# Kernel tuning notes

Measured on AMD Instinct MI355X. Metric: run time of the kernel, lower is better.

## Reference

```python
import jax, jax.numpy as jnp
import numpy as np
from jax import lax

B, L, H, E, V = 16, 128, 1024, 512, 32000
MAX_LENGTH = 128
SOS_INDEX = 1
NUM_LAYERS = 2


def setup_inputs() -> dict:
    key = jax.random.key(0)
    ks = jax.random.split(key, 16)
    inp = {}
    inp['input_tensor'] = jax.random.randint(ks[0], (B, L), 0, V)
    inp['target_tensor'] = jax.random.randint(ks[1], (B, L), 0, V)
    inp['true_sample'] = 1
    s = lambda k, shape, fan: jax.random.normal(k, shape, jnp.float32) / np.float32(np.sqrt(fan))
    inp['embedding'] = jax.random.normal(ks[2], (V, E), jnp.float32) * 0.02
    inp['enc_W'] = s(ks[3], (E, H), E)
    inp['enc_b'] = jnp.zeros((H,), jnp.float32)
    inp['Wih0'] = s(ks[4], (E, 3 * H), E)
    inp['Whh0'] = s(ks[5], (H, 3 * H), H)
    inp['bih0'] = jnp.zeros((3 * H,), jnp.float32)
    inp['bhh0'] = jnp.zeros((3 * H,), jnp.float32)
    inp['Wih1'] = s(ks[6], (H, 3 * H), H)
    inp['Whh1'] = s(ks[7], (H, 3 * H), H)
    inp['bih1'] = jnp.zeros((3 * H,), jnp.float32)
    inp['bhh1'] = jnp.zeros((3 * H,), jnp.float32)
    inp['W_out'] = s(ks[8], (2 * H, V), 2 * H)
    inp['b_out'] = jnp.zeros((V,), jnp.float32)
    return inp


def _gru_cell(x, h, Wih, Whh, bih, bhh):
    gx = x @ Wih + bih
    gh = h @ Whh + bhh
    xr, xz, xn = jnp.split(gx, 3, axis=-1)
    hr, hz, hn = jnp.split(gh, 3, axis=-1)
    r = jax.nn.sigmoid(xr + hr)
    z = jax.nn.sigmoid(xz + hz)
    n = jnp.tanh(xn + r * hn)
    return (1.0 - z) * n + z * h


def _forward(input_tensor, true_sample, embedding, enc_W, enc_b,
             Wih0, Whh0, bih0, bhh0, Wih1, Whh1, bih1, bhh1, W_out, b_out):
    batch_size, input_length = input_tensor.shape
    target_length = input_length
    # Encoder: embed + per-timestep projection -> [B, L, H]
    enc_emb = embedding[input_tensor]
    enc_hidden = jnp.tanh(enc_emb @ enc_W + enc_b)
    enc_hidden_t = jnp.transpose(enc_hidden, (1, 0, 2))  # [L, B, H]
    # Pad at the front to max_length (mirrors the copy loop)
    encoder_outputs = jnp.zeros((MAX_LENGTH, batch_size, H), enc_hidden.dtype)
    encoder_outputs = encoder_outputs.at[MAX_LENGTH - input_length:].set(enc_hidden_t)
    # Decoder initial hidden: last encoder state stacked over layers
    h_init = enc_hidden_t[-1]  # [B, H]
    # NOTE: original never updates decoder_input inside the loop -> constant SOS
    x0 = jnp.broadcast_to(embedding[SOS_INDEX], (batch_size, E))
    inv_sqrt_h = np.float32(1.0 / np.sqrt(H))

    def step(carry, _):
        h0, h1 = carry
        h0 = _gru_cell(x0, h0, Wih0, Whh0, bih0, bhh0)
        h1 = _gru_cell(h0, h1, Wih1, Whh1, bih1, bhh1)
        scores = jnp.einsum('bh,lbh->bl', h1, encoder_outputs) * inv_sqrt_h
        attn = jax.nn.softmax(scores, axis=-1)
        ctx = jnp.einsum('bl,lbh->bh', attn, encoder_outputs)
        logits = jnp.concatenate([h1, ctx], axis=-1) @ W_out + b_out
        return (h0, h1), jax.nn.sigmoid(logits)

    _, probs = lax.scan(step, (h_init, h_init), None, length=target_length)
    decoder_outputs = jnp.transpose(probs, (1, 0, 2))  # [B, T, V]
    # Scalar gather: p[b,w] = decoder_outputs[b, w, input_tensor[b, w]]
    out_probabilities = jnp.take_along_axis(decoder_outputs, input_tensor[..., None], axis=2)[..., 0]
    target = jnp.full(input_tensor.shape, np.float32(int(true_sample)), jnp.float32)
    p = jnp.clip(out_probabilities, 1e-12, 1.0 - 1e-7)
    bce = -(target * jnp.log(p) + (1.0 - target) * jnp.log1p(-p))
    loss = jnp.mean(bce) / np.float32(batch_size)
    return loss, out_probabilities


def reference(input_tensor, target_tensor, true_sample, embedding, enc_W, enc_b,
              Wih0, Whh0, bih0, bhh0, Wih1, Whh1, bih1, bhh1, W_out, b_out):
    return _forward(input_tensor, true_sample, embedding, enc_W, enc_b,
                    Wih0, Whh0, bih0, bhh0, Wih1, Whh1, bih1, bhh1, W_out, b_out)
```

## Files before the change

### kernel.cpp

```cpp
#include <hip/hip_runtime.h>
#include <math.h>

#define BB 16
#define LL 128
#define HH 1024
#define EE 512
#define VV 32000
#define G3 3072
#define NBLK 256

__device__ __forceinline__ float sigmoidf_(float x){ return 1.0f/(1.0f+expf(-x)); }

__global__ void k_rowidx(const int* __restrict__ inp, int* __restrict__ idx){
  int r = blockIdx.x*256 + threadIdx.x;
  if (r < 2048){ int l = r >> 4, b = r & 15; idx[r] = inp[b*LL + l]; }
}

template<int ACT, int KK>
__global__ __launch_bounds__(256) void k_gemm(const float* __restrict__ A, const int* __restrict__ rowidx,
                       const float* __restrict__ Bm, const float* __restrict__ bias,
                       float* __restrict__ C, int N){
  constexpr int KS = (KK==512)?9:10;
  __shared__ float As[32*KK];
  const int tid = threadIdx.x;
  const int r0 = blockIdx.x*32;
  const int c  = blockIdx.y*512 + (tid<<1);
  for (int i = tid; i < 32*KK; i += 256){
    int rr = i >> KS;
    int row = r0 + rr;
    int arow = rowidx ? rowidx[row] : row;
    int kk = i - (rr<<KS);
    As[i] = A[(size_t)arow*KK + kk];
  }
  __syncthreads();
  float2 acc[32];
  #pragma unroll
  for (int r=0;r<32;r++){ acc[r].x=0.f; acc[r].y=0.f; }
  for (int k=0;k<KK;k++){
    const float2 w = *(const float2*)(Bm + (size_t)k*N + c);
    #pragma unroll
    for (int r=0;r<32;r++){
      float a = As[(r<<KS)+k];
      acc[r].x = fmaf(a,w.x,acc[r].x);
      acc[r].y = fmaf(a,w.y,acc[r].y);
    }
  }
  const float2 bv = *(const float2*)(bias + c);
  #pragma unroll
  for (int r=0;r<32;r++){
    float x = acc[r].x + bv.x, y = acc[r].y + bv.y;
    if (ACT==1){ x = tanhf(x); y = tanhf(y); }
    *(float2*)(C + (size_t)(r0+r)*N + c) = make_float2(x,y);
  }
}

__global__ __launch_bounds__(256,1) void k_chains(
    const float* enclast, float* H0all, float* H1all,
    const float* __restrict__ Whh0, const float* __restrict__ Whh1,
    const float* __restrict__ Wih0, const float* __restrict__ Wih1,
    const float* __restrict__ emb,
    const float* __restrict__ bih0, const float* __restrict__ bhh0,
    const float* __restrict__ bhh1, const float* __restrict__ bih1,
    int* flags, int* go)
{
  __shared__ float w0l[12][1024];
  __shared__ float w1l[12][1024];
  __shared__ float wil[12][1024];
  const int tid  = threadIdx.x;
  const int lane = tid & 63;
  const int bc   = tid >> 6;
  const int kl   = lane & 15;
  const int cg   = lane >> 4;
  const int jb   = blockIdx.x << 2;
  const int b    = (bc << 2) + cg;
  const int jp_  = jb + kl;
  const bool act = (kl < 4);

  float g0r=0.f, g0z=0.f, g0n=0.f;
  {
    for (int idx = tid; idx < 1536; idx += 256){
      int g = idx >> 9, k = idx & 511;
      float4 a = *(const float4*)(Wih0 + (size_t)k*G3 + g*1024 + jb);
      w0l[g*4+0][k]=a.x; w0l[g*4+1][k]=a.y; w0l[g*4+2][k]=a.z; w0l[g*4+3][k]=a.w;
    }
    __syncthreads();
    const float* e1 = emb + EE;
    float ag[12];
    #pragma unroll
    for (int c=0;c<12;c++) ag[c]=0.f;
    #pragma unroll
    for (int i=0;i<8;i++){
      float4 e = *(const float4*)(e1 + i*64 + (kl<<2));
      #pragma unroll
      for (int c=0;c<12;c++){
        const float4 w = *(const float4*)(&w0l[c][i*64 + (kl<<2)]);
        float v = ag[c];
        v=fmaf(w.x,e.x,v); v=fmaf(w.y,e.y,v); v=fmaf(w.z,e.z,v); v=fmaf(w.w,e.w,v);
        ag[c]=v;
      }
    }
    #pragma unroll
    for (int c=0;c<12;c++){
      float v = ag[c];
      v+=__shfl_xor(v,1,64); v+=__shfl_xor(v,2,64);
      v+=__shfl_xor(v,4,64); v+=__shfl_xor(v,8,64);
      ag[c]=v;
    }
    if (act){
      float sr=0.f, sz=0.f, sn=0.f;
      #pragma unroll
      for (int jj=0;jj<4;jj++){
        bool sel = (kl==jj);
        sr = sel ? ag[jj]   : sr;
        sz = sel ? ag[4+jj] : sz;
        sn = sel ? ag[8+jj] : sn;
      }
      g0r = sr + bih0[jp_];
      g0z = sz + bih0[1024+jp_];
      g0n = sn + bih0[2048+jp_];
    }
    __syncthreads();
  }

  for (int idx = tid; idx < 3072; idx += 256){
    int g = idx >> 10, k = idx & 1023;
    float4 a = *(const float4*)(Whh0 + (size_t)k*G3 + g*1024 + jb);
    w0l[g*4+0][k]=a.x; w0l[g*4+1][k]=a.y; w0l[g*4+2][k]=a.z; w0l[g*4+3][k]=a.w;
    float4 d = *(const float4*)(Whh1 + (size_t)k*G3 + g*1024 + jb);
    w1l[g*4+0][k]=d.x; w1l[g*4+1][k]=d.y; w1l[g*4+2][k]=d.z; w1l[g*4+3][k]=d.w;
    float4 e = *(const float4*)(Wih1 + (size_t)k*G3 + g*1024 + jb);
    wil[g*4+0][k]=e.x; wil[g*4+1][k]=e.y; wil[g*4+2][k]=e.z; wil[g*4+3][k]=e.w;
  }
  float b0r_=0.f,b0z_=0.f,b0n_=0.f,b1r_=0.f,b1z_=0.f,b1n_=0.f,bir_=0.f,biz_=0.f,bin_=0.f;
  if (act){
    b0r_ = bhh0[jp_]; b0z_ = bhh0[1024+jp_]; b0n_ = bhh0[2048+jp_];
    b1r_ = bhh1[jp_]; b1z_ = bhh1[1024+jp_]; b1n_ = bhh1[2048+jp_];
    bir_ = bih1[jp_]; biz_ = bih1[1024+jp_]; bin_ = bih1[2048+jp_];
  }
  __syncthreads();

  for (int t = 0; t <= LL; ++t){
    const float* hp0 = (t==0) ? enclast : (H0all + (size_t)(t-1)*(BB*HH));
    const float* hp1 = (t<=1) ? enclast : (H1all + (size_t)(t-2)*(BB*HH));
    float hprev0 = 0.f, hprev1 = 0.f;
    if (act){
      hprev0 = hp0[(size_t)b*HH + jp_];
      hprev1 = hp1[(size_t)b*HH + jp_];
    }

    float acc0[12], accg[12];
    #pragma unroll
    for (int c=0;c<12;c++){ acc0[c]=0.f; accg[c]=0.f; }
    {
      const float* hrow = hp0 + (size_t)b*HH;
      for (int i=0;i<16;i++){
        float4 hv = *(const float4*)(hrow + i*64 + (kl<<2));
        #pragma unroll
        for (int c=0;c<12;c++){
          const float4 wa = *(const float4*)(&w0l[c][i*64 + (kl<<2)]);
          float v = acc0[c];
          v=fmaf(wa.x,hv.x,v); v=fmaf(wa.y,hv.y,v); v=fmaf(wa.z,hv.z,v); v=fmaf(wa.w,hv.w,v);
          acc0[c]=v;
          const float4 wg = *(const float4*)(&wil[c][i*64 + (kl<<2)]);
          float u = accg[c];
          u=fmaf(wg.x,hv.x,u); u=fmaf(wg.y,hv.y,u); u=fmaf(wg.z,hv.z,u); u=fmaf(wg.w,hv.w,u);
          accg[c]=u;
        }
      }
    }
    #pragma unroll
    for (int c=0;c<12;c++){
      float v = acc0[c];
      v+=__shfl_xor(v,1,64); v+=__shfl_xor(v,2,64);
      v+=__shfl_xor(v,4,64); v+=__shfl_xor(v,8,64);
      acc0[c]=v;
      float u = accg[c];
      u+=__shfl_xor(u,1,64); u+=__shfl_xor(u,2,64);
      u+=__shfl_xor(u,4,64); u+=__shfl_xor(u,8,64);
      accg[c]=u;
    }

    if (t < LL && act){
      float ghr=0.f, ghz=0.f, ghn=0.f;
      #pragma unroll
      for (int jj=0;jj<4;jj++){
        bool sel = (kl==jj);
        ghr = sel ? acc0[jj]   : ghr;
        ghz = sel ? acc0[4+jj] : ghz;
        ghn = sel ? acc0[8+jj] : ghn;
      }
      float r = sigmoidf_(g0r + ghr + b0r_);
      float z = sigmoidf_(g0z + ghz + b0z_);
      float n = tanhf    (g0n + r*(ghn + b0n_));
      float hnew = (1.f-z)*n + z*hprev0;
      __hip_atomic_store((int*)&H0all[(size_t)t*(BB*HH) + (size_t)b*HH + jp_],
                         __float_as_int(hnew),
                         __ATOMIC_RELAXED, __HIP_MEMORY_SCOPE_AGENT);
    }

    if (t >= 1){
      float acc1[12];
      #pragma unroll
      for (int c=0;c<12;c++) acc1[c]=0.f;
      const float* hrow = hp1 + (size_t)b*HH;
      for (int i=0;i<16;i++){
        float4 hv = *(const float4*)(hrow + i*64 + (kl<<2));
        #pragma unroll
        for (int c=0;c<12;c++){
          const float4 w = *(const float4*)(&w1l[c][i*64 + (kl<<2)]);
          float v = acc1[c];
          v=fmaf(w.x,hv.x,v); v=fmaf(w.y,hv.y,v); v=fmaf(w.z,hv.z,v); v=fmaf(w.w,hv.w,v);
          acc1[c]=v;
        }
      }
      #pragma unroll
      for (int c=0;c<12;c++){
        float v = acc1[c];
        v+=__shfl_xor(v,1,64); v+=__shfl_xor(v,2,64);
        v+=__shfl_xor(v,4,64); v+=__shfl_xor(v,8,64);
        acc1[c]=v;
      }
      if (act){
        float ghr=0.f, ghz=0.f, ghn=0.f, gxr=0.f, gxz=0.f, gxn=0.f;
        #pragma unroll
        for (int jj=0;jj<4;jj++){
          bool sel = (kl==jj);
          ghr = sel ? acc1[jj]   : ghr;
          ghz = sel ? acc1[4+jj] : ghz;
          ghn = sel ? acc1[8+jj] : ghn;
          gxr = sel ? accg[jj]   : gxr;
          gxz = sel ? accg[4+jj] : gxz;
          gxn = sel ? accg[8+jj] : gxn;
        }
        float r = sigmoidf_(gxr + bir_ + ghr + b1r_);
        float z = sigmoidf_(gxz + biz_ + ghz + b1z_);
        float n = tanhf    (gxn + bin_ + r*(ghn + b1n_));
        float hnew = (1.f-z)*n + z*hprev1;
        __hip_atomic_store((int*)&H1all[(size_t)(t-1)*(BB*HH) + (size_t)b*HH + jp_],
                           __float_as_int(hnew),
                           __ATOMIC_RELAXED, __HIP_MEMORY_SCOPE_AGENT);
      }
    }

    if (t < LL){
      const int val = t + 1;
      asm volatile("s_waitcnt vmcnt(0)" ::: "memory");
      __syncthreads();
      if (tid == 0)
        __hip_atomic_store(&flags[(int)blockIdx.x*32], val,
                           __ATOMIC_RELAXED, __HIP_MEMORY_SCOPE_AGENT);
      if (blockIdx.x == 0){
        while (__hip_atomic_load(&flags[tid*32], __ATOMIC_RELAXED,
                                 __HIP_MEMORY_SCOPE_AGENT) < val)
          __builtin_amdgcn_s_sleep(1);
        __syncthreads();
        if (tid == 0)
          __hip_atomic_store(go, val, __ATOMIC_RELAXED, __HIP_MEMORY_SCOPE_AGENT);
      } else {
        if (tid == 0){
          while (__hip_atomic_load(go, __ATOMIC_RELAXED,
                                   __HIP_MEMORY_SCOPE_AGENT) < val)
            __builtin_amdgcn_s_sleep(1);
        }
        __syncthreads();
      }
    }
  }
}

__global__ __launch_bounds__(256) void k_attn(const float* __restrict__ enc, const float* __restrict__ H1,
                       float* __restrict__ ctx){
  __shared__ float h1s[8][HH];
  __shared__ float sc[8][LL];
  __shared__ float part[2][8][LL];
  const int tid = threadIdx.x;
  const int s0 = blockIdx.x*8, b = blockIdx.y;
  for (int i = tid; i < 8*HH; i += 256){
    int si = i >> 10, k = i & 1023;
    h1s[si][k] = H1[(size_t)(s0+si)*BB*HH + (size_t)b*HH + k];
  }
  __syncthreads();
  {
    const int l = tid & 127, half = tid >> 7;
    const float4* er = (const float4*)(enc + ((size_t)l*BB + b)*HH + half*512);
    float a[8];
    #pragma unroll
    for (int s=0;s<8;s++) a[s]=0.f;
    for (int q=0;q<128;q++){
      float4 e = er[q];
      #pragma unroll
      for (int s=0;s<8;s++){
        const float4 h = *(const float4*)(&h1s[s][half*512 + q*4]);
        a[s] += h.x*e.x + h.y*e.y + h.z*e.z + h.w*e.w;
      }
    }
    #pragma unroll
    for (int s=0;s<8;s++) part[half][s][l] = a[s];
  }
  __syncthreads();
  for (int p = tid; p < 1024; p += 256){
    int s = p >> 7, l = p & 127;
    sc[s][l] = (part[0][s][l] + part[1][s][l]) * 0.03125f;
  }
  __syncthreads();
  {
    int s = tid >> 5, lid = tid & 31;
    float v0 = sc[s][lid], v1 = sc[s][lid+32], v2 = sc[s][lid+64], v3 = sc[s][lid+96];
    float m = fmaxf(fmaxf(v0,v1),fmaxf(v2,v3));
    for (int off=16; off>=1; off>>=1) m = fmaxf(m, __shfl_xor(m, off, 32));
    float e0=__expf(v0-m), e1=__expf(v1-m), e2=__expf(v2-m), e3=__expf(v3-m);
    float ssum = e0+e1+e2+e3;
    for (int off=16; off>=1; off>>=1) ssum += __shfl_xor(ssum, off, 32);
    float inv = 1.0f/ssum;
    sc[s][lid]=e0*inv; sc[s][lid+32]=e1*inv; sc[s][lid+64]=e2*inv; sc[s][lid+96]=e3*inv;
  }
  __syncthreads();
  {
    float acc[4][8];
    #pragma unroll
    for (int q=0;q<4;q++)
      #pragma unroll
      for (int s=0;s<8;s++) acc[q][s]=0.f;
    for (int l=0;l<128;l++){
      const float* er = enc + ((size_t)l*BB + b)*HH + tid;
      float a[8];
      #pragma unroll
      for (int s=0;s<8;s++) a[s] = sc[s][l];
      #pragma unroll
      for (int q=0;q<4;q++){
        float e = er[q*256];
        #pragma unroll
        for (int s=0;s<8;s++) acc[q][s] = fmaf(a[s], e, acc[q][s]);
      }
    }
    #pragma unroll
    for (int s=0;s<8;s++)
      #pragma unroll
      for (int q=0;q<4;q++)
        ctx[(size_t)(s0+s)*BB*HH + (size_t)b*HH + tid + q*256] = acc[q][s];
  }
}

__global__ __launch_bounds__(256) void k_logit(const float* __restrict__ H1, const float* __restrict__ ctx,
                        const float* __restrict__ Wout, const float* __restrict__ bout,
                        const int* __restrict__ inp, const int* __restrict__ ts,
                        float* __restrict__ outp, float* __restrict__ bce){
  __shared__ float rbuf[256];
  const int i = blockIdx.x;
  const int b = i >> 7, t = i & 127;
  const int v = inp[b*LL + t];
  const int tid = threadIdx.x;
  const float* h1r = H1 + ((size_t)t*BB + b)*HH;
  const float* cxr = ctx + ((size_t)t*BB + b)*HH;
  float acc = 0.f;
  #pragma unroll
  for (int q=0;q<4;q++){
    int k = tid + q*256;
    acc = fmaf(h1r[k], Wout[(size_t)k*VV + v], acc);
  }
  #pragma unroll
  for (int q=0;q<4;q++){
    int k = tid + q*256;
    acc = fmaf(cxr[k], Wout[(size_t)(k+1024)*VV + v], acc);
  }
  rbuf[tid] = acc;
  __syncthreads();
  for (int s=128; s>0; s>>=1){
    if (tid < s) rbuf[tid] += rbuf[tid+s];
    __syncthreads();
  }
  if (tid==0){
    float logit = rbuf[0] + bout[v];
    float p = 1.0f/(1.0f + expf(-logit));
    outp[b*LL + t] = p;
    float pc = fminf(fmaxf(p, 1e-12f), 1.0f - 1e-7f);
    float tg = (float)ts[0];
    bce[i] = -(tg*logf(pc) + (1.0f-tg)*log1pf(-pc));
  }
}

__global__ void k_loss(const float* __restrict__ bce, float* __restrict__ out0){
  __shared__ float rbuf[256];
  int tid = threadIdx.x;
  float s = 0.f;
  for (int i = tid; i < 2048; i += 256) s += bce[i];
  rbuf[tid] = s; __syncthreads();
  for (int st=128; st>0; st>>=1){
    if (tid<st) rbuf[tid]+=rbuf[tid+st];
    __syncthreads();
  }
  if (tid==0) out0[0] = rbuf[0] * (1.0f/(2048.0f*16.0f));
}

extern "C" void kernel_launch(void* const* d_in, const int* in_sizes, int n_in,
                              void* d_out, int out_size, void* d_ws, size_t ws_size,
                              hipStream_t stream){
  (void)in_sizes; (void)n_in; (void)out_size; (void)ws_size;
  const int*   inp   = (const int*)d_in[0];
  const int*   ts    = (const int*)d_in[2];
  const float* emb   = (const float*)d_in[3];
  const float* encW  = (const float*)d_in[4];
  const float* encb  = (const float*)d_in[5];
  const float* Wih0  = (const float*)d_in[6];
  const float* Whh0  = (const float*)d_in[7];
  const float* bih0  = (const float*)d_in[8];
  const float* bhh0  = (const float*)d_in[9];
  const float* Wih1  = (const float*)d_in[10];
  const float* Whh1  = (const float*)d_in[11];
  const float* bih1  = (const float*)d_in[12];
  const float* bhh1  = (const float*)d_in[13];
  const float* Wout  = (const float*)d_in[14];
  const float* bout  = (const float*)d_in[15];
  float* out = (float*)d_out;

  float* ws      = (float*)d_ws;
  float* enc_out = ws;
  float* H0      = enc_out + 2097152;
  float* H1      = H0 + 2097152;
  float* GX1     = H1 + 2097152;
  float* CTX     = GX1 + 6291456;
  float* gx0     = CTX + 2097152;
  float* bceb    = gx0 + 3072;
  int*   rowidx  = (int*)(bceb + 2048);
  int*   flags   = rowidx + 2048;
  int*   go      = flags + 256*32;

  hipMemsetAsync(flags, 0, (256*32 + 32)*sizeof(int), stream);
  k_rowidx<<<8,256,0,stream>>>(inp, rowidx);
  k_gemm<1,512><<<dim3(64,2),256,0,stream>>>(emb, rowidx, encW, encb, enc_out, HH);

  const float* enclast = enc_out + (size_t)127*BB*HH;

  k_chains<<<NBLK,256,0,stream>>>(enclast, H0, H1, Whh0, Whh1, Wih0, Wih1, emb,
                                  bih0, bhh0, bhh1, bih1, flags, go);
  k_attn<<<dim3(16,16),256,0,stream>>>(enc_out, H1, CTX);
  k_logit<<<2048,256,0,stream>>>(H1, CTX, Wout, bout, inp, ts, out+1, bceb);
  k_loss<<<1,256,0,stream>>>(bceb, out);
}
```

Before: 2.251 ms.

## Split GRU chain step into two phases with decentralized all-to-all flag barriers

The persistent recurrent kernel now runs 512 threads per block, with 32 lanes per batch row over the K dimension. Each timestep is split into two phases: layer 1 (including the Wih1 projection of layer-0 output) and then layer 0, each followed by its own flag. The centralized barrier, where block 0 gathered all flags and released a go flag, is replaced by every block polling all 256 per-block flags directly. This removes one hop of barrier latency per step and doubles the threads doing the per-step dot products. The cost is an extra barrier per step and heavier polling traffic on the flag array.

```diff
diff --git a/kernel.cpp b/kernel.cpp
--- a/kernel.cpp
+++ b/kernel.cpp
@@ -10,6 +10,13 @@
 #define NBLK 256
 
 __device__ __forceinline__ float sigmoidf_(float x){ return 1.0f/(1.0f+expf(-x)); }
+
+__device__ __forceinline__ float redk(float v){
+  v += __shfl_xor(v, 1, 64); v += __shfl_xor(v, 2, 64);
+  v += __shfl_xor(v, 4, 64); v += __shfl_xor(v, 8, 64);
+  v += __shfl_xor(v, 16, 64);
+  return v;
+}
 
 __global__ void k_rowidx(const int* __restrict__ inp, int* __restrict__ idx){
   int r = blockIdx.x*256 + threadIdx.x;
@@ -54,31 +61,32 @@
   }
 }
 
-__global__ __launch_bounds__(256,1) void k_chains(
+__global__ __launch_bounds__(512,1) void k_chains(
     const float* enclast, float* H0all, float* H1all,
     const float* __restrict__ Whh0, const float* __restrict__ Whh1,
     const float* __restrict__ Wih0, const float* __restrict__ Wih1,
     const float* __restrict__ emb,
     const float* __restrict__ bih0, const float* __restrict__ bhh0,
     const float* __restrict__ bhh1, const float* __restrict__ bih1,
-    int* flags, int* go)
+    int* flagsB, int* flagsA)
 {
   __shared__ float w0l[12][1024];
   __shared__ float w1l[12][1024];
   __shared__ float wil[12][1024];
   const int tid  = threadIdx.x;
   const int lane = tid & 63;
-  const int bc   = tid >> 6;
-  const int kl   = lane & 15;
-  const int cg   = lane >> 4;
+  const int wv   = tid >> 6;
+  const int kl   = lane & 31;
+  const int bh   = lane >> 5;
   const int jb   = blockIdx.x << 2;
-  const int b    = (bc << 2) + cg;
+  const int b    = (wv << 1) + bh;
   const int jp_  = jb + kl;
   const bool act = (kl < 4);
+  const int koff = kl << 2;
 
   float g0r=0.f, g0z=0.f, g0n=0.f;
   {
-    for (int idx = tid; idx < 1536; idx += 256){
+    for (int idx = tid; idx < 1536; idx += 512){
       int g = idx >> 9, k = idx & 511;
       float4 a = *(const float4*)(Wih0 + (size_t)k*G3 + g*1024 + jb);
       w0l[g*4+0][k]=a.x; w0l[g*4+1][k]=a.y; w0l[g*4+2][k]=a.z; w0l[g*4+3][k]=a.w;
@@ -89,23 +97,18 @@
     #pragma unroll
     for (int c=0;c<12;c++) ag[c]=0.f;
     #pragma unroll
-    for (int i=0;i<8;i++){
-      float4 e = *(const float4*)(e1 + i*64 + (kl<<2));
+    for (int i=0;i<4;i++){
+      float4 e = *(const float4*)(e1 + i*128 + koff);
       #pragma unroll
       for (int c=0;c<12;c++){
-        const float4 w = *(const float4*)(&w0l[c][i*64 + (kl<<2)]);
+        const float4 w = *(const float4*)(&w0l[c][i*128 + koff]);
         float v = ag[c];
         v=fmaf(w.x,e.x,v); v=fmaf(w.y,e.y,v); v=fmaf(w.z,e.z,v); v=fmaf(w.w,e.w,v);
         ag[c]=v;
       }
     }
     #pragma unroll
-    for (int c=0;c<12;c++){
-      float v = ag[c];
-      v+=__shfl_xor(v,1,64); v+=__shfl_xor(v,2,64);
-      v+=__shfl_xor(v,4,64); v+=__shfl_xor(v,8,64);
-      ag[c]=v;
-    }
+    for (int c=0;c<12;c++) ag[c] = redk(ag[c]);
     if (act){
       float sr=0.f, sz=0.f, sn=0.f;
       #pragma unroll
@@ -122,7 +125,7 @@
     __syncthreads();
   }
 
-  for (int idx = tid; idx < 3072; idx += 256){
+  for (int idx = tid; idx < 3072; idx += 512){
     int g = idx >> 10, k = idx & 1023;
     float4 a = *(const float4*)(Whh0 + (size_t)k*G3 + g*1024 + jb);
     w0l[g*4+0][k]=a.x; w0l[g*4+1][k]=a.y; w0l[g*4+2][k]=a.z; w0l[g*4+3][k]=a.w;
@@ -139,87 +142,45 @@
   }
   __syncthreads();
 
-  for (int t = 0; t <= LL; ++t){
-    const float* hp0 = (t==0) ? enclast : (H0all + (size_t)(t-1)*(BB*HH));
-    const float* hp1 = (t<=1) ? enclast : (H1all + (size_t)(t-2)*(BB*HH));
-    float hprev0 = 0.f, hprev1 = 0.f;
-    if (act){
-      hprev0 = hp0[(size_t)b*HH + jp_];
-      hprev1 = hp1[(size_t)b*HH + jp_];
-    }
-
-    float acc0[12], accg[12];
-    #pragma unroll
-    for (int c=0;c<12;c++){ acc0[c]=0.f; accg[c]=0.f; }
-    {
-      const float* hrow = hp0 + (size_t)b*HH;
-      for (int i=0;i<16;i++){
-        float4 hv = *(const float4*)(hrow + i*64 + (kl<<2));
+  const int myflag = (int)blockIdx.x * 32;
+  const int pollfl = (tid & 255) * 32;
+
+  for (int t = 0; t <= LL+1; ++t){
+    if (t >= 1){
+      while (__hip_atomic_load(&flagsB[pollfl], __ATOMIC_RELAXED,
+                               __HIP_MEMORY_SCOPE_AGENT) < t)
+        __builtin_amdgcn_s_sleep(1);
+      __syncthreads();
+    }
+
+    if (t >= 2){
+      const float* h0row = H0all + (size_t)(t-2)*(BB*HH) + (size_t)b*HH;
+      const float* h1row = ((t==2) ? enclast : (H1all + (size_t)(t-3)*(BB*HH)))
+                           + (size_t)b*HH;
+      float hprev1 = 0.f;
+      if (act) hprev1 = h1row[kl];
+      if (act) hprev1 = h1row[jp_];
+      float accg[12], acc1[12];
+      #pragma unroll
+      for (int c=0;c<12;c++){ accg[c]=0.f; acc1[c]=0.f; }
+      #pragma unroll
+      for (int i=0;i<8;i++){
+        float4 h0v = *(const float4*)(h0row + i*128 + koff);
+        float4 h1v = *(const float4*)(h1row + i*128 + koff);
         #pragma unroll
         for (int c=0;c<12;c++){
-          const float4 wa = *(const float4*)(&w0l[c][i*64 + (kl<<2)]);
-          float v = acc0[c];
-          v=fmaf(wa.x,hv.x,v); v=fmaf(wa.y,hv.y,v); v=fmaf(wa.z,hv.z,v); v=fmaf(wa.w,hv.w,v);
-          acc0[c]=v;
-          const float4 wg = *(const float4*)(&wil[c][i*64 + (kl<<2)]);
+          const float4 wg = *(const float4*)(&wil[c][i*128 + koff]);
           float u = accg[c];
-          u=fmaf(wg.x,hv.x,u); u=fmaf(wg.y,hv.y,u); u=fmaf(wg.z,hv.z,u); u=fmaf(wg.w,hv.w,u);
+          u=fmaf(wg.x,h0v.x,u); u=fmaf(wg.y,h0v.y,u); u=fmaf(wg.z,h0v.z,u); u=fmaf(wg.w,h0v.w,u);
           accg[c]=u;
-        }
-      }
-    }
-    #pragma unroll
-    for (int c=0;c<12;c++){
-      float v = acc0[c];
-      v+=__shfl_xor(v,1,64); v+=__shfl_xor(v,2,64);
-      v+=__shfl_xor(v,4,64); v+=__shfl_xor(v,8,64);
-      acc0[c]=v;
-      float u = accg[c];
-      u+=__shfl_xor(u,1,64); u+=__shfl_xor(u,2,64);
-      u+=__shfl_xor(u,4,64); u+=__shfl_xor(u,8,64);
-      accg[c]=u;
-    }
-
-    if (t < LL && act){
-      float ghr=0.f, ghz=0.f, ghn=0.f;
-      #pragma unroll
-      for (int jj=0;jj<4;jj++){
-        bool sel = (kl==jj);
-        ghr = sel ? acc0[jj]   : ghr;
-        ghz = sel ? acc0[4+jj] : ghz;
-        ghn = sel ? acc0[8+jj] : ghn;
-      }
-      float r = sigmoidf_(g0r + ghr + b0r_);
-      float z = sigmoidf_(g0z + ghz + b0z_);
-      float n = tanhf    (g0n + r*(ghn + b0n_));
-      float hnew = (1.f-z)*n + z*hprev0;
-      __hip_atomic_store((int*)&H0all[(size_t)t*(BB*HH) + (size_t)b*HH + jp_],
-                         __float_as_int(hnew),
-                         __ATOMIC_RELAXED, __HIP_MEMORY_SCOPE_AGENT);
-    }
-
-    if (t >= 1){
-      float acc1[12];
-      #pragma unroll
-      for (int c=0;c<12;c++) acc1[c]=0.f;
-      const float* hrow = hp1 + (size_t)b*HH;
-      for (int i=0;i<16;i++){
-        float4 hv = *(const float4*)(hrow + i*64 + (kl<<2));
-        #pragma unroll
-        for (int c=0;c<12;c++){
-          const float4 w = *(const float4*)(&w1l[c][i*64 + (kl<<2)]);
+          const float4 w1 = *(const float4*)(&w1l[c][i*128 + koff]);
           float v = acc1[c];
-          v=fmaf(w.x,hv.x,v); v=fmaf(w.y,hv.y,v); v=fmaf(w.z,hv.z,v); v=fmaf(w.w,hv.w,v);
+          v=fmaf(w1.x,h1v.x,v); v=fmaf(w1.y,h1v.y,v); v=fmaf(w1.z,h1v.z,v); v=fmaf(w1.w,h1v.w,v);
           acc1[c]=v;
         }
       }
       #pragma unroll
-      for (int c=0;c<12;c++){
-        float v = acc1[c];
-        v+=__shfl_xor(v,1,64); v+=__shfl_xor(v,2,64);
-        v+=__shfl_xor(v,4,64); v+=__shfl_xor(v,8,64);
-        acc1[c]=v;
-      }
+      for (int c=0;c<12;c++){ accg[c] = redk(accg[c]); acc1[c] = redk(acc1[c]); }
       if (act){
         float ghr=0.f, ghz=0.f, ghn=0.f, gxr=0.f, gxz=0.f, gxn=0.f;
         #pragma unroll
@@ -236,35 +197,70 @@
         float z = sigmoidf_(gxz + biz_ + ghz + b1z_);
         float n = tanhf    (gxn + bin_ + r*(ghn + b1n_));
         float hnew = (1.f-z)*n + z*hprev1;
-        __hip_atomic_store((int*)&H1all[(size_t)(t-1)*(BB*HH) + (size_t)b*HH + jp_],
+        __hip_atomic_store((int*)&H1all[(size_t)(t-2)*(BB*HH) + (size_t)b*HH + jp_],
                            __float_as_int(hnew),
                            __ATOMIC_RELAXED, __HIP_MEMORY_SCOPE_AGENT);
       }
     }
 
+    asm volatile("s_waitcnt vmcnt(0)" ::: "memory");
+    __syncthreads();
+    if (tid == 0)
+      __hip_atomic_store(&flagsB[myflag], t+1,
+                         __ATOMIC_RELAXED, __HIP_MEMORY_SCOPE_AGENT);
+
+    if (t >= 1){
+      while (__hip_atomic_load(&flagsA[pollfl], __ATOMIC_RELAXED,
+                               __HIP_MEMORY_SCOPE_AGENT) < t)
+        __builtin_amdgcn_s_sleep(1);
+      __syncthreads();
+    }
+
     if (t < LL){
-      const int val = t + 1;
-      asm volatile("s_waitcnt vmcnt(0)" ::: "memory");
-      __syncthreads();
-      if (tid == 0)
-        __hip_atomic_store(&flags[(int)blockIdx.x*32], val,
+      const float* h0row = ((t==0) ? enclast : (H0all + (size_t)(t-1)*(BB*HH)))
+                           + (size_t)b*HH;
+      float hprev0 = 0.f;
+      if (act) hprev0 = h0row[jp_];
+      float acc0[12];
+      #pragma unroll
+      for (int c=0;c<12;c++) acc0[c]=0.f;
+      #pragma unroll
+      for (int i=0;i<8;i++){
+        float4 hv = *(const float4*)(h0row + i*128 + koff);
+        #pragma unroll
+        for (int c=0;c<12;c++){
+          const float4 w = *(const float4*)(&w0l[c][i*128 + koff]);
+          float v = acc0[c];
+          v=fmaf(w.x,hv.x,v); v=fmaf(w.y,hv.y,v); v=fmaf(w.z,hv.z,v); v=fmaf(w.w,hv.w,v);
+          acc0[c]=v;
+        }
+      }
+      #pragma unroll
+      for (int c=0;c<12;c++) acc0[c] = redk(acc0[c]);
+      if (act){
+        float ghr=0.f, ghz=0.f, ghn=0.f;
+        #pragma unroll
+        for (int jj=0;jj<4;jj++){
+          bool sel = (kl==jj);
+          ghr = sel ? acc0[jj]   : ghr;
+          ghz = sel ? acc0[4+jj] : ghz;
+          ghn = sel ? acc0[8+jj] : ghn;
+        }
+        float r = sigmoidf_(g0r + ghr + b0r_);
+        float z = sigmoidf_(g0z + ghz + b0z_);
+        float n = tanhf    (g0n + r*(ghn + b0n_));
+        float hnew = (1.f-z)*n + z*hprev0;
+        __hip_atomic_store((int*)&H0all[(size_t)t*(BB*HH) + (size_t)b*HH + jp_],
+                           __float_as_int(hnew),
                            __ATOMIC_RELAXED, __HIP_MEMORY_SCOPE_AGENT);
-      if (blockIdx.x == 0){
-        while (__hip_atomic_load(&flags[tid*32], __ATOMIC_RELAXED,
-                                 __HIP_MEMORY_SCOPE_AGENT) < val)
-          __builtin_amdgcn_s_sleep(1);
-        __syncthreads();
-        if (tid == 0)
-          __hip_atomic_store(go, val, __ATOMIC_RELAXED, __HIP_MEMORY_SCOPE_AGENT);
-      } else {
-        if (tid == 0){
-          while (__hip_atomic_load(go, __ATOMIC_RELAXED,
-                                   __HIP_MEMORY_SCOPE_AGENT) < val)
-            __builtin_amdgcn_s_sleep(1);
-        }
-        __syncthreads();
-      }
-    }
+      }
+    }
+
+    asm volatile("s_waitcnt vmcnt(0)" ::: "memory");
+    __syncthreads();
+    if (tid == 0)
+      __hip_atomic_store(&flagsA[myflag], t+1,
+                         __ATOMIC_RELAXED, __HIP_MEMORY_SCOPE_AGENT);
   }
 }
 
@@ -422,17 +418,17 @@
   float* gx0     = CTX + 2097152;
   float* bceb    = gx0 + 3072;
   int*   rowidx  = (int*)(bceb + 2048);
-  int*   flags   = rowidx + 2048;
-  int*   go      = flags + 256*32;
-
-  hipMemsetAsync(flags, 0, (256*32 + 32)*sizeof(int), stream);
+  int*   flagsB  = rowidx + 2048;
+  int*   flagsA  = flagsB + 256*32;
+
+  hipMemsetAsync(flagsB, 0, 512*32*sizeof(int), stream);
   k_rowidx<<<8,256,0,stream>>>(inp, rowidx);
   k_gemm<1,512><<<dim3(64,2),256,0,stream>>>(emb, rowidx, encW, encb, enc_out, HH);
 
   const float* enclast = enc_out + (size_t)127*BB*HH;
 
-  k_chains<<<NBLK,256,0,stream>>>(enclast, H0, H1, Whh0, Whh1, Wih0, Wih1, emb,
-                                  bih0, bhh0, bhh1, bih1, flags, go);
+  k_chains<<<NBLK,512,0,stream>>>(enclast, H0, H1, Whh0, Whh1, Wih0, Wih1, emb,
+                                  bih0, bhh0, bhh1, bih1, flagsB, flagsA);
   k_attn<<<dim3(16,16),256,0,stream>>>(enc_out, H1, CTX);
   k_logit<<<2048,256,0,stream>>>(H1, CTX, Wout, bout, inp, ts, out+1, bceb);
   k_loss<<<1,256,0,stream>>>(bceb, out);
```

Result: faster. 2.079 ms (-7.6%).
